# Optimization experiments

Hardware: AMD Instinct MI355X
Metric: run time of the kernel (lower is better)

The kernel has to match this reference:

```python
import jax, jax.numpy as jnp
import numpy as np

MARGIN = 1.0
EPS = 1e-12


def setup_inputs() -> dict:
    key = jax.random.key(0)
    k1, k2, k3 = jax.random.split(key, 3)
    B, C, D = 16384, 500, 512
    features = jax.random.normal(k1, (B, D), dtype=jnp.float32)
    prototypes = jax.random.normal(k2, (C, D), dtype=jnp.float32)
    labels = jax.random.randint(k3, (B,), 0, C, dtype=jnp.int64)
    return {"features": features, "prototypes": prototypes, "labels": labels}


def reference(features, prototypes, labels):
    # Pairwise L2 distances [B, C] via the expanded form (no [B,C,D] intermediate)
    f2 = jnp.sum(features * features, axis=-1, keepdims=True)   # [B, 1]
    p2 = jnp.sum(prototypes * prototypes, axis=-1)               # [C]
    sq = f2 + p2 - 2.0 * (features @ prototypes.T)               # [B, C]
    dists = jnp.sqrt(jnp.maximum(sq, EPS))                       # [B, C]

    B, C = dists.shape
    d_pos = jnp.take_along_axis(dists, labels[:, None], axis=1)[:, 0]  # [B]
    pos_mask = jax.nn.one_hot(labels, C, dtype=bool)             # [B, C]
    d_neg_min = jnp.min(jnp.where(pos_mask, jnp.inf, dists), axis=-1)  # [B]

    loss = jnp.mean(jax.nn.relu(d_pos - d_neg_min + MARGIN))
    return loss
```

## Files before the change

kernel.cpp:

```cpp
#include <hip/hip_runtime.h>
#include <stdint.h>
#include <stddef.h>

#define BB 16384
#define CC 500
#define DD 512
#define PADC 512
#define LMARGIN 1.0f
#define EPSQ 1e-12f
#define NK 16
#define ROWS 32

typedef __attribute__((ext_vector_type(8))) _Float16 f16x8;
typedef __attribute__((ext_vector_type(4))) _Float16 f16x4;
typedef __attribute__((ext_vector_type(4))) float f32x4;

__global__ void prepP_kernel(const float* __restrict__ protos,
                             unsigned short* __restrict__ protoT,
                             float* __restrict__ p2,
                             float* __restrict__ out) {
  __shared__ float s_arr[16][17];
  const int cg = blockIdx.x;
  const int t = threadIdx.x;
  const int colin = t & 15;
  const int jb = t >> 4;
  const int col = cg * 16 + colin;
  if (cg == 0 && t == 0) out[0] = 0.f;
  float s = 0.f;
#pragma unroll
  for (int u = 0; u < 4; ++u) {
    const int j8 = jb + u * 16;
    const int kc = j8 >> 2, quad = j8 & 3;
    f32x4 a0 = {0.f, 0.f, 0.f, 0.f}, a1 = a0;
    if (col < CC) {
      const float* src = protos + (size_t)col * DD + j8 * 8;
      a0 = *(const f32x4*)src;
      a1 = *(const f32x4*)(src + 4);
    }
    f16x8 h;
#pragma unroll
    for (int uu = 0; uu < 4; ++uu) {
      h[uu] = (_Float16)a0[uu];
      h[uu + 4] = (_Float16)a1[uu];
      s = fmaf(a0[uu], a0[uu], s);
      s = fmaf(a1[uu], a1[uu], s);
    }
    *(f16x8*)(protoT + (size_t)(cg * 16 + kc) * 512 + (quad * 16 + colin) * 8) = h;
  }
  s_arr[colin][jb] = s;
  __syncthreads();
  if (t < 16) {
    float acc = 0.f;
#pragma unroll
    for (int i = 0; i < 16; ++i) acc += s_arr[t][i];
    p2[cg * 16 + t] = acc;
  }
}

__launch_bounds__(512, 4)
__global__ void main_kernel(const float* __restrict__ feat,
                            const unsigned short* __restrict__ protoT,
                            const float* __restrict__ p2,
                            const int* __restrict__ labels,
                            float* __restrict__ outp) {
  __shared__ __align__(16) unsigned char Afull[NK * 2048];
  float* redM = (float*)&Afull[0];
  float* redP = (float*)&Afull[1024];
  float* f2l = (float*)&Afull[2048];

  const int tid = threadIdx.x;
  const int w = tid >> 6;
  const int lane = tid & 63;
  const int lane16 = lane & 15;
  const int quad = lane >> 4;
  const int r0 = blockIdx.x * ROWS;
  const int rot = (blockIdx.x >> 3) & 15;

  const char* bptr[4];
#pragma unroll
  for (int nt = 0; nt < 4; ++nt)
    bptr[nt] = (const char*)protoT + (size_t)(w * 64 + nt * 16) * 1024 + lane * 16;

  f16x8 bfr[3][4];
#pragma unroll
  for (int nt = 0; nt < 4; ++nt) {
    bfr[0][nt] = *(const f16x8*)(bptr[nt] + (size_t)rot * 1024);
    bfr[1][nt] = *(const f16x8*)(bptr[nt] + (size_t)((rot + 1) & 15) * 1024);
  }

  const int arow = tid >> 4;
  const int aj = tid & 15;
  const int aj7 = aj & 7, ajh = aj >> 3;
  const float* aSrc = feat + (size_t)(r0 + arow) * DD + aj * 4;
  const int awbase =
      arow * 64 + (((aj7 >> 1) ^ ((arow >> 1) & 3)) * 16) + (aj7 & 1) * 8;

  float s = 0.f;
  {
    f32x4 av[8];
#pragma unroll
    for (int i = 0; i < 8; ++i) av[i] = *(const f32x4*)(aSrc + i * 64);
#pragma unroll
    for (int i = 0; i < 8; ++i) {
      f16x4 h;
#pragma unroll
      for (int u = 0; u < 4; ++u) {
        h[u] = (_Float16)av[i][u];
        s = fmaf(av[i][u], av[i][u], s);
      }
      *(f16x4*)(&Afull[(2 * i + ajh) * 2048 + awbase]) = h;
    }
  }
  s += __shfl_xor(s, 1, 64);
  s += __shfl_xor(s, 2, 64);
  s += __shfl_xor(s, 4, 64);
  s += __shfl_xor(s, 8, 64);

  f32x4 acc[2][4];
#pragma unroll
  for (int mt = 0; mt < 2; ++mt)
#pragma unroll
    for (int nt = 0; nt < 4; ++nt) acc[mt][nt] = (f32x4){0.f, 0.f, 0.f, 0.f};

  __syncthreads();

  const int aroff = lane16 * 64 + ((quad ^ ((lane16 >> 1) & 3)) * 16);
#pragma unroll
  for (int kc = 0; kc < NK; ++kc) {
    const int kr = (kc + rot) & 15;
    if (kc + 2 < NK) {
      const int kp = (kc + 2 + rot) & 15;
#pragma unroll
      for (int nt = 0; nt < 4; ++nt)
        bfr[(kc + 2) % 3][nt] = *(const f16x8*)(bptr[nt] + (size_t)kp * 1024);
    }
    f16x8 af[2];
#pragma unroll
    for (int mt = 0; mt < 2; ++mt)
      af[mt] = *(const f16x8*)(&Afull[kr * 2048 + mt * 1024 + aroff]);
#pragma unroll
    for (int mt = 0; mt < 2; ++mt)
#pragma unroll
      for (int nt = 0; nt < 4; ++nt)
        acc[mt][nt] = __builtin_amdgcn_mfma_f32_16x16x32_f16(
            af[mt], bfr[kc % 3][nt], acc[mt][nt], 0, 0, 0);
  }

  __syncthreads();

  if ((tid & 15) == 0) f2l[arow] = s;

  float p2v[4];
#pragma unroll
  for (int nt = 0; nt < 4; ++nt) p2v[nt] = p2[w * 64 + nt * 16 + lane16];

#pragma unroll
  for (int mt = 0; mt < 2; ++mt) {
#pragma unroll
    for (int i = 0; i < 4; ++i) {
      const int row = mt * 16 + quad * 4 + i;
      const int lb = labels[r0 + row];
      float qm = 1e30f, qp = -1e30f;
#pragma unroll
      for (int nt = 0; nt < 4; ++nt) {
        const int col = w * 64 + nt * 16 + lane16;
        float q = p2v[nt] - 2.f * acc[mt][nt][i];
        bool isPos = (col == lb);
        qp = fmaxf(qp, isPos ? q : -1e30f);
        qm = fminf(qm, (!isPos && col < CC) ? q : 1e30f);
      }
#pragma unroll
      for (int d = 1; d < 16; d <<= 1) {
        qm = fminf(qm, __shfl_xor(qm, d, 64));
        qp = fmaxf(qp, __shfl_xor(qp, d, 64));
      }
      if (lane16 == 0) {
        redM[row * 8 + w] = qm;
        redP[row * 8 + w] = qp;
      }
    }
  }
  __syncthreads();

  if (tid < ROWS) {
    float qm = 1e30f, qp = -1e30f;
#pragma unroll
    for (int j = 0; j < 8; ++j) {
      qm = fminf(qm, redM[tid * 8 + j]);
      qp = fmaxf(qp, redP[tid * 8 + j]);
    }
    float f2 = f2l[tid];
    float dn = sqrtf(fmaxf(f2 + qm, EPSQ));
    float dp = sqrtf(fmaxf(f2 + qp, EPSQ));
    float term = fmaxf(dp - dn + LMARGIN, 0.f);
#pragma unroll
    for (int d = 1; d < 32; d <<= 1) term += __shfl_xor(term, d, 64);
    if (tid == 0) atomicAdd(outp, term * (1.0f / BB));
  }
}

extern "C" void kernel_launch(void* const* d_in, const int* in_sizes, int n_in,
                              void* d_out, int out_size, void* d_ws, size_t ws_size,
                              hipStream_t stream) {
  const float* feat = (const float*)d_in[0];
  const float* protos = (const float*)d_in[1];
  const int* labels = (const int*)d_in[2];
  float* out = (float*)d_out;

  char* ws = (char*)d_ws;
  unsigned short* protoT = (unsigned short*)(ws);
  float* p2 = (float*)(ws + (512 << 10));

  prepP_kernel<<<32, 256, 0, stream>>>(protos, protoT, p2, out);
  main_kernel<<<BB / ROWS, 512, 0, stream>>>(feat, protoT, p2, labels, out);
}
```

Before: 93.61 us.

## Stream fp32 feature tiles into LDS via async global_load_lds, convert at fragment load

Replaces the register-staged feature load (global load, convert to fp16, LDS store, then one barrier) with direct global-to-LDS DMA of fp32 rows in four quarter-K stages, overlapped with the MFMA loop. The fp16 conversion now happens when A fragments are read from LDS, and the feature row norms are computed from the fp32 LDS copy after the GEMM. It also drops the per-block k-rotation of prototype loads. The aim is to overlap feature loading with compute and cut the register and VALU cost of staging, at the price of doubling LDS use to 64KB, which may reduce occupancy, and adding more barriers and conversion work inside the loop.

```diff
diff --git a/kernel.cpp b/kernel.cpp
--- a/kernel.cpp
+++ b/kernel.cpp
@@ -8,12 +8,19 @@
 #define PADC 512
 #define LMARGIN 1.0f
 #define EPSQ 1e-12f
-#define NK 16
+#define NKC 16
 #define ROWS 32
 
 typedef __attribute__((ext_vector_type(8))) _Float16 f16x8;
 typedef __attribute__((ext_vector_type(4))) _Float16 f16x4;
 typedef __attribute__((ext_vector_type(4))) float f32x4;
+
+#define GLOBAL_AS __attribute__((address_space(1)))
+#define LDS_AS __attribute__((address_space(3)))
+
+__device__ __forceinline__ void ld_lds16(const void* g, void* l) {
+  __builtin_amdgcn_global_load_lds((const GLOBAL_AS void*)g, (LDS_AS void*)l, 16, 0, 0);
+}
 
 __global__ void prepP_kernel(const float* __restrict__ protos,
                              unsigned short* __restrict__ protoT,
@@ -63,10 +70,10 @@
                             const float* __restrict__ p2,
                             const int* __restrict__ labels,
                             float* __restrict__ outp) {
-  __shared__ __align__(16) unsigned char Afull[NK * 2048];
-  float* redM = (float*)&Afull[0];
-  float* redP = (float*)&Afull[1024];
-  float* f2l = (float*)&Afull[2048];
+  __shared__ __align__(16) unsigned char Afp[NKC * 4096];
+  float* redM = (float*)&Afp[0];
+  float* redP = (float*)&Afp[1024];
+  float* f2l = (float*)&Afp[2048];
 
   const int tid = threadIdx.x;
   const int w = tid >> 6;
@@ -74,7 +81,6 @@
   const int lane16 = lane & 15;
   const int quad = lane >> 4;
   const int r0 = blockIdx.x * ROWS;
-  const int rot = (blockIdx.x >> 3) & 15;
 
   const char* bptr[4];
 #pragma unroll
@@ -84,71 +90,92 @@
   f16x8 bfr[3][4];
 #pragma unroll
   for (int nt = 0; nt < 4; ++nt) {
-    bfr[0][nt] = *(const f16x8*)(bptr[nt] + (size_t)rot * 1024);
-    bfr[1][nt] = *(const f16x8*)(bptr[nt] + (size_t)((rot + 1) & 15) * 1024);
-  }
-
-  const int arow = tid >> 4;
-  const int aj = tid & 15;
-  const int aj7 = aj & 7, ajh = aj >> 3;
-  const float* aSrc = feat + (size_t)(r0 + arow) * DD + aj * 4;
-  const int awbase =
-      arow * 64 + (((aj7 >> 1) ^ ((arow >> 1) & 3)) * 16) + (aj7 & 1) * 8;
+    bfr[0][nt] = *(const f16x8*)(bptr[nt]);
+    bfr[1][nt] = *(const f16x8*)(bptr[nt] + 1024);
+  }
+
+  const int l3 = lane >> 3, j8 = lane & 7;
+  const float* aBase = feat + (size_t)(r0 + l3) * DD + ((j8 ^ l3) << 2);
+  char* ldsBase = (char*)Afp + lane * 16;
+  const int kcq0 = w >> 2, rb0 = w & 3;
+  const int kcq1 = (8 + w) >> 2, rb1 = (8 + w) & 3;
+
+#define DMA_Q(q)                                                            \
+  do {                                                                      \
+    int kcA = (q) * 4 + kcq0, kcB = (q) * 4 + kcq1;                         \
+    ld_lds16(aBase + (size_t)(rb0 * 8) * DD + kcA * 32,                     \
+             ldsBase + kcA * 4096 + rb0 * 1024);                            \
+    ld_lds16(aBase + (size_t)(rb1 * 8) * DD + kcB * 32,                     \
+             ldsBase + kcB * 4096 + rb1 * 1024);                            \
+  } while (0)
+
+  DMA_Q(0);
+
+  f32x4 acc[2][4];
+#pragma unroll
+  for (int mt = 0; mt < 2; ++mt)
+#pragma unroll
+    for (int nt = 0; nt < 4; ++nt) acc[mt][nt] = (f32x4){0.f, 0.f, 0.f, 0.f};
+
+  __syncthreads();
+
+  const int r7 = lane16 & 7;
+  const int c0 = ((quad * 2) ^ r7) * 16;
+  const int c1 = ((quad * 2 + 1) ^ r7) * 16;
+#pragma unroll
+  for (int qi = 0; qi < 4; ++qi) {
+    if (qi < 3) DMA_Q(qi + 1);
+#pragma unroll
+    for (int j = 0; j < 4; ++j) {
+      const int kc = qi * 4 + j;
+      if (kc + 2 < NKC) {
+#pragma unroll
+        for (int nt = 0; nt < 4; ++nt)
+          bfr[(kc + 2) % 3][nt] =
+              *(const f16x8*)(bptr[nt] + (size_t)(kc + 2) * 1024);
+      }
+      f16x8 af[2];
+#pragma unroll
+      for (int mt = 0; mt < 2; ++mt) {
+        const unsigned char* ab = Afp + kc * 4096 + (mt * 16 + lane16) * 128;
+        f32x4 x0 = *(const f32x4*)(ab + c0);
+        f32x4 x1 = *(const f32x4*)(ab + c1);
+        f16x8 a;
+#pragma unroll
+        for (int u = 0; u < 4; ++u) {
+          a[u] = (_Float16)x0[u];
+          a[u + 4] = (_Float16)x1[u];
+        }
+        af[mt] = a;
+      }
+#pragma unroll
+      for (int mt = 0; mt < 2; ++mt)
+#pragma unroll
+        for (int nt = 0; nt < 4; ++nt)
+          acc[mt][nt] = __builtin_amdgcn_mfma_f32_16x16x32_f16(
+              af[mt], bfr[kc % 3][nt], acc[mt][nt], 0, 0, 0);
+    }
+    if (qi < 3) __syncthreads();
+  }
+#undef DMA_Q
 
   float s = 0.f;
   {
-    f32x4 av[8];
-#pragma unroll
-    for (int i = 0; i < 8; ++i) av[i] = *(const f32x4*)(aSrc + i * 64);
-#pragma unroll
-    for (int i = 0; i < 8; ++i) {
-      f16x4 h;
-#pragma unroll
-      for (int u = 0; u < 4; ++u) {
-        h[u] = (_Float16)av[i][u];
-        s = fmaf(av[i][u], av[i][u], s);
-      }
-      *(f16x4*)(&Afull[(2 * i + ajh) * 2048 + awbase]) = h;
-    }
-  }
-  s += __shfl_xor(s, 1, 64);
-  s += __shfl_xor(s, 2, 64);
-  s += __shfl_xor(s, 4, 64);
-  s += __shfl_xor(s, 8, 64);
-
-  f32x4 acc[2][4];
-#pragma unroll
-  for (int mt = 0; mt < 2; ++mt)
-#pragma unroll
-    for (int nt = 0; nt < 4; ++nt) acc[mt][nt] = (f32x4){0.f, 0.f, 0.f, 0.f};
-
-  __syncthreads();
-
-  const int aroff = lane16 * 64 + ((quad ^ ((lane16 >> 1) & 3)) * 16);
-#pragma unroll
-  for (int kc = 0; kc < NK; ++kc) {
-    const int kr = (kc + rot) & 15;
-    if (kc + 2 < NK) {
-      const int kp = (kc + 2 + rot) & 15;
-#pragma unroll
-      for (int nt = 0; nt < 4; ++nt)
-        bfr[(kc + 2) % 3][nt] = *(const f16x8*)(bptr[nt] + (size_t)kp * 1024);
-    }
-    f16x8 af[2];
-#pragma unroll
-    for (int mt = 0; mt < 2; ++mt)
-      af[mt] = *(const f16x8*)(&Afull[kr * 2048 + mt * 1024 + aroff]);
-#pragma unroll
-    for (int mt = 0; mt < 2; ++mt)
-#pragma unroll
-      for (int nt = 0; nt < 4; ++nt)
-        acc[mt][nt] = __builtin_amdgcn_mfma_f32_16x16x32_f16(
-            af[mt], bfr[kc % 3][nt], acc[mt][nt], 0, 0, 0);
-  }
-
-  __syncthreads();
-
-  if ((tid & 15) == 0) f2l[arow] = s;
+    const int frow = tid >> 4, fkc = tid & 15, t7 = tid & 7;
+    const unsigned char* fb = Afp + fkc * 4096 + frow * 128;
+#pragma unroll
+    for (int si = 0; si < 8; ++si) {
+      const int slot = ((si + t7) & 7) * 16;
+      f32x4 v = *(const f32x4*)(fb + slot);
+      s = fmaf(v[0], v[0], fmaf(v[1], v[1], fmaf(v[2], v[2], fmaf(v[3], v[3], s))));
+    }
+    s += __shfl_xor(s, 1, 64);
+    s += __shfl_xor(s, 2, 64);
+    s += __shfl_xor(s, 4, 64);
+    s += __shfl_xor(s, 8, 64);
+  }
+  __syncthreads();
+  if ((tid & 15) == 0) f2l[tid >> 4] = s;
 
   float p2v[4];
 #pragma unroll
```

New measurement: 94.82 us. Within noise of the previous version (+1.3%).
